# Kernel tuning notes

Measured on AMD Instinct MI355X. Metric: run time of the kernel, lower is better.

The kernel has to match this reference:

```python
import jax, jax.numpy as jnp
import numpy as np

B, N = 1, 768
C_A, C_S, C_Z = 768, 384, 128
H, C_HID, N_TRANS = 16, 48, 2
INF = 1e9
PNAMES = ['attn_s_ln_g', 'attn_ada_gate_w', 'attn_ada_gate_b', 'attn_ada_skip_w',
          'wq', 'bq', 'wk', 'wv', 'z_ln_g', 'z_ln_b', 'wb', 'wg', 'wo',
          'attn_out_gate_w', 'attn_out_gate_b',
          'tr_s_ln_g', 'tr_ada_gate_w', 'tr_ada_gate_b', 'tr_ada_skip_w',
          'tr_w1', 'tr_w2', 'tr_wo', 'tr_out_gate_w', 'tr_out_gate_b']


def _ln(x, eps=1e-5):
    mu = jnp.mean(x, axis=-1, keepdims=True)
    var = jnp.mean((x - mu) ** 2, axis=-1, keepdims=True)
    return (x - mu) * jax.lax.rsqrt(var + eps)


def _adaln(a, s, s_g, gate_w, gate_b, skip_w):
    # AF3 Algorithm 26 AdaLN: a <- LN(a, no affine); s <- LN(s, scale only)
    a_ln = _ln(a)
    s_ln = _ln(s) * s_g
    return jax.nn.sigmoid(s_ln @ gate_w + gate_b) * a_ln + s_ln @ skip_w


def setup_inputs() -> dict:
    key = jax.random.key(0)
    ks = iter(jax.random.split(key, 40))
    w = lambda *sh: jax.random.normal(next(ks), sh, jnp.float32) * 0.02
    return dict(
        a=jax.random.normal(next(ks), (B, N, C_A), jnp.float32),
        s=jax.random.normal(next(ks), (B, N, C_S), jnp.float32),
        z=jax.random.normal(next(ks), (B, N, N, C_Z), jnp.float32),
        mask=jnp.ones((B, N), jnp.int32),
        attn_s_ln_g=jnp.ones((C_S,), jnp.float32),
        attn_ada_gate_w=w(C_S, C_A),
        attn_ada_gate_b=jnp.zeros((C_A,), jnp.float32),
        attn_ada_skip_w=w(C_S, C_A),
        wq=w(C_A, H * C_HID), bq=jnp.zeros((H * C_HID,), jnp.float32),
        wk=w(C_A, H * C_HID), wv=w(C_A, H * C_HID),
        z_ln_g=jnp.ones((C_Z,), jnp.float32), z_ln_b=jnp.zeros((C_Z,), jnp.float32),
        wb=w(C_Z, H), wg=w(C_A, H * C_HID), wo=w(H * C_HID, C_A),
        attn_out_gate_w=w(C_S, C_A),
        attn_out_gate_b=jnp.full((C_A,), -2.0, jnp.float32),  # AdaLN-Zero bias init -2
        tr_s_ln_g=jnp.ones((C_S,), jnp.float32),
        tr_ada_gate_w=w(C_S, C_A),
        tr_ada_gate_b=jnp.zeros((C_A,), jnp.float32),
        tr_ada_skip_w=w(C_S, C_A),
        tr_w1=w(C_A, N_TRANS * C_A), tr_w2=w(C_A, N_TRANS * C_A),
        tr_wo=w(N_TRANS * C_A, C_A),
        tr_out_gate_w=w(C_S, C_A),
        tr_out_gate_b=jnp.full((C_A,), -2.0, jnp.float32),
    )


def _block(a, s, z, maskf, p):
    # --- AttentionPairBias (AF3 Alg 24), residual ---
    a_ln = _adaln(a, s, p['attn_s_ln_g'], p['attn_ada_gate_w'],
                  p['attn_ada_gate_b'], p['attn_ada_skip_w'])
    q = (a_ln @ p['wq'] + p['bq']).reshape(B, N, H, C_HID)
    k = (a_ln @ p['wk']).reshape(B, N, H, C_HID)
    v = (a_ln @ p['wv']).reshape(B, N, H, C_HID)
    pair_bias = (_ln(z) * p['z_ln_g'] + p['z_ln_b']) @ p['wb']  # [B,N,N,H]
    logits = jnp.einsum('bqhc,bkhc->bhqk', q, k) / np.float32(np.sqrt(C_HID))
    logits = logits + jnp.moveaxis(pair_bias, -1, 1)
    logits = logits + (maskf - 1.0)[:, None, None, :] * INF  # mask over keys
    attn = jax.nn.softmax(logits, axis=-1)
    o = jnp.einsum('bhqk,bkhc->bqhc', attn, v)
    g = jax.nn.sigmoid(a_ln @ p['wg']).reshape(B, N, H, C_HID)
    o = (o * g).reshape(B, N, H * C_HID) @ p['wo']
    o = jax.nn.sigmoid(s @ p['attn_out_gate_w'] + p['attn_out_gate_b']) * o
    a = a + o
    # --- ConditionedTransitionBlock (AF3 Alg 25, SwiGLU), residual ---
    t_ln = _adaln(a, s, p['tr_s_ln_g'], p['tr_ada_gate_w'],
                  p['tr_ada_gate_b'], p['tr_ada_skip_w'])
    hid = jax.nn.silu(t_ln @ p['tr_w1']) * (t_ln @ p['tr_w2'])
    t = jax.nn.sigmoid(s @ p['tr_out_gate_w'] + p['tr_out_gate_b']) * (hid @ p['tr_wo'])
    t = t * maskf[..., None]  # _mask_trans=True
    return a + t


def reference(a, s, z, mask, attn_s_ln_g, attn_ada_gate_w, attn_ada_gate_b,
              attn_ada_skip_w, wq, bq, wk, wv, z_ln_g, z_ln_b, wb, wg, wo,
              attn_out_gate_w, attn_out_gate_b, tr_s_ln_g, tr_ada_gate_w,
              tr_ada_gate_b, tr_ada_skip_w, tr_w1, tr_w2, tr_wo,
              tr_out_gate_w, tr_out_gate_b):
    p = dict(zip(PNAMES, (attn_s_ln_g, attn_ada_gate_w, attn_ada_gate_b,
                          attn_ada_skip_w, wq, bq, wk, wv, z_ln_g, z_ln_b, wb,
                          wg, wo, attn_out_gate_w, attn_out_gate_b, tr_s_ln_g,
                          tr_ada_gate_w, tr_ada_gate_b, tr_ada_skip_w, tr_w1,
                          tr_w2, tr_wo, tr_out_gate_w, tr_out_gate_b)))
    return _block(a, s, z, mask.astype(a.dtype), p)
```

## Files before the change

### kernel.cpp

```cpp
#include <hip/hip_runtime.h>
#include <hip/hip_bf16.h>
#include <stdint.h>


typedef __bf16 bf16x8 __attribute__((ext_vector_type(8)));
typedef float  f32x4  __attribute__((ext_vector_type(4)));

#define DEVI __device__ __forceinline__

DEVI uint16_t f2b(float f){ __hip_bfloat16 h = __float2bfloat16(f); return __builtin_bit_cast(uint16_t, h); }
DEVI float    b2f(uint16_t u){ return __bfloat162float(__builtin_bit_cast(__hip_bfloat16, u)); }
DEVI float    sigm(float x){ return 1.0f/(1.0f + __expf(-x)); }

DEVI f32x4 MFMA(uint4 a, uint4 b, f32x4 c){
  return __builtin_amdgcn_mfma_f32_16x16x32_bf16(
      __builtin_bit_cast(bf16x8, a), __builtin_bit_cast(bf16x8, b), c, 0, 0, 0);
}

DEVI void glds16(const void* g, void* l){
  __builtin_amdgcn_global_load_lds(
      (const __attribute__((address_space(1))) void*)g,
      (__attribute__((address_space(3))) void*)l, 16, 0, 0);
}

constexpr size_t SZ_BT_ADA   = (size_t)1536*384*2;
constexpr size_t OFF_BT_ADA_ATTN = 0;
constexpr size_t OFF_BT_ADA_TR   = OFF_BT_ADA_ATTN + SZ_BT_ADA;
constexpr size_t OFF_BT_OUTGATE  = OFF_BT_ADA_TR   + SZ_BT_ADA;
constexpr size_t OFF_BT_QKVG     = OFF_BT_OUTGATE  + SZ_BT_ADA;
constexpr size_t OFF_BT_WO       = OFF_BT_QKVG + (size_t)3072*768*2;
constexpr size_t OFF_BT_W12      = OFF_BT_WO   + (size_t)768*768*2;
constexpr size_t OFF_BT_TRWO     = OFF_BT_W12  + (size_t)3072*768*2;
constexpr size_t OFF_WBGT        = OFF_BT_TRWO + (size_t)768*1536*2;
constexpr size_t OFF_ZCOL        = OFF_WBGT + 4096;
constexpr size_t OFF_OGB         = OFF_ZCOL + 256;
constexpr size_t OFF_SBF         = OFF_OGB + 6144;
constexpr size_t OFF_SLNA        = OFF_SBF  + (size_t)768*384*2;
constexpr size_t OFF_SLNT        = OFF_SLNA + (size_t)768*384*2;
constexpr size_t OFF_GATEOUT     = OFF_SLNT + (size_t)768*384*2;
constexpr size_t OFF_LNA         = OFF_GATEOUT + (size_t)768*1536*4;
constexpr size_t OFF_GST         = OFF_LNA + (size_t)768*1536*4;
constexpr size_t OFF_ALNBF       = OFF_GST + (size_t)768*1536*4;
constexpr size_t OFF_QP          = OFF_ALNBF + (size_t)768*768*2;
constexpr size_t OFF_KP          = OFF_QP + (size_t)16*768*48*2;
constexpr size_t OFF_VT          = OFF_KP + (size_t)16*768*48*2;
constexpr size_t OFF_GB          = OFF_VT + (size_t)16*48*768*2;
constexpr size_t OFF_BIASB       = OFF_GB + (size_t)768*768*2;
constexpr size_t OFF_OBF         = OFF_BIASB + (size_t)16*768*768*2;
constexpr size_t OFF_AMID        = OFF_OBF + (size_t)768*768*2;
constexpr size_t OFF_HID         = OFF_BIASB;

extern "C" size_t kernel_workspace_size(void){ return (size_t)64 << 20; }

DEVI void cvt_body(const float* src, uint16_t* dst, int K, int N, int il, int local,
                   float (*lds)[33])
{
  int t = threadIdx.x;
  int tN = N >> 5;
  int n0 = (local % tN) << 5, k0 = (local / tN) << 5;
  int c = t & 31, r0 = t >> 5;
  #pragma unroll
  for (int i = 0; i < 4; i++){
    int kk = r0 + 8*i;
    lds[kk][c] = src[(size_t)(k0+kk)*N + n0 + c];
  }
  __syncthreads();
  int rbase = (il == 0) ? n0 : (((n0 >> 5) << 6) + ((il == 2) ? 32 : 0));
  #pragma unroll
  for (int i = 0; i < 4; i++){
    int nn = r0 + 8*i;
    dst[(size_t)(rbase+nn)*K + k0 + c] = f2b(lds[c][nn]);
  }
}

struct PreArgs {
  const float* src[6];
  uint16_t*    dst[6];
  int K[6], N[6], il[6];
  int prefix[7];
  int n_cvt;
  const float *s, *g_attn, *g_tr, *aogb, *togb, *zg, *zb, *wb, *ain;
  uint16_t *s_bf, *sln_a, *sln_t, *lna;
  float* ogb; uint16_t* wbgt; float* zcol;
};

__global__ __launch_bounds__(256) void k_pre(PreArgs a){
  __shared__ float lds[32][33];
  __shared__ float rs_[4], rq_[4];
  int bid = blockIdx.x, t = threadIdx.x;
  if (bid < a.n_cvt){
    int ti = 0;
    while (ti < 5 && bid >= a.prefix[ti+1]) ti++;
    cvt_body(a.src[ti], a.dst[ti], a.K[ti], a.N[ti], a.il[ti], bid - a.prefix[ti], lds);
    return;
  }
  int b = bid - a.n_cvt;
  if (b < 384){
    int row_id = b*2 + (t >> 7);
    int tt = t & 127;
    const float* row = a.s + (size_t)row_id*384;
    float x0 = row[tt], x1 = row[tt+128], x2 = row[tt+256];
    float sm = x0+x1+x2, sq = x0*x0+x1*x1+x2*x2;
    #pragma unroll
    for (int off = 32; off; off >>= 1){ sm += __shfl_xor(sm, off, 64); sq += __shfl_xor(sq, off, 64); }
    int w = t >> 6;
    if ((t & 63) == 0){ rs_[w] = sm; rq_[w] = sq; }
    __syncthreads();
    int base = (t >> 7)*2;
    float S = rs_[base]+rs_[base+1], Q = rq_[base]+rq_[base+1];
    float mu = S * (1.f/384.f);
    float var = Q * (1.f/384.f) - mu*mu;
    float rstd = rsqrtf(var + 1e-5f);
    float xs[3] = {x0, x1, x2};
    #pragma unroll
    for (int i = 0; i < 3; i++){
      int ci = tt + 128*i;
      float ln = (xs[i] - mu) * rstd;
      a.s_bf [(size_t)row_id*384 + ci] = f2b(xs[i]);
      a.sln_a[(size_t)row_id*384 + ci] = f2b(ln * a.g_attn[ci]);
      a.sln_t[(size_t)row_id*384 + ci] = f2b(ln * a.g_tr[ci]);
    }
  } else if (b == 384){
    for (int i = t; i < 1536; i += 256)
      a.ogb[i] = (i < 768) ? a.aogb[i] : a.togb[i-768];
  } else if (b == 385){
    for (int i = t; i < 2048; i += 256){
      int h = i >> 7, c = i & 127;
      a.wbgt[i] = f2b(a.zg[c] * a.wb[c*16 + h]);
    }
    if (t < 16){
      float cs = 0.f, cn = 0.f;
      for (int c = 0; c < 128; c++){ cs += a.zg[c]*a.wb[c*16+t]; cn += a.zb[c]*a.wb[c*16+t]; }
      a.zcol[t] = cs; a.zcol[16+t] = cn;
    }
  } else {
    int row = b - 386;
    const float* rp = a.ain + (size_t)row*768;
    float x0 = rp[t], x1 = rp[t+256], x2 = rp[t+512];
    float sm = x0+x1+x2, sq = x0*x0+x1*x1+x2*x2;
    #pragma unroll
    for (int off = 32; off; off >>= 1){ sm += __shfl_xor(sm, off, 64); sq += __shfl_xor(sq, off, 64); }
    int w = t >> 6;
    if ((t & 63) == 0){ rs_[w] = sm; rq_[w] = sq; }
    __syncthreads();
    float S = rs_[0]+rs_[1]+rs_[2]+rs_[3], Q = rq_[0]+rq_[1]+rq_[2]+rq_[3];
    float mu = S*(1.f/768.f), var = Q*(1.f/768.f) - mu*mu, rstd = rsqrtf(var + 1e-5f);
    float xs[3] = {x0, x1, x2};
    #pragma unroll
    for (int i = 0; i < 3; i++)
      a.lna[(size_t)row*768 + t + 256*i] = f2b((xs[i]-mu)*rstd);
  }
}

struct GemmP {
  const uint16_t *A, *BT;
  int N, K, gx, mode, gateLd, gateOff;
  float* outF; uint16_t* outB;
  const float *bias, *resid;
  const uint16_t *gate, *lna;
  const int* mask;
  uint16_t *qp, *kp, *vt, *gb;
  const float* bq;
};

DEVI void gemm_body(const GemmP& p, int bx, int by, uint16_t* As, uint16_t* Bs){
  int t = threadIdx.x;
  int n0 = bx*64, m0 = by*64;
  int w = t >> 6, lane = t & 63, mm = lane & 15, q = lane >> 4;
  const uint16_t* gA[4]; const uint16_t* gB[4];
  uint16_t* lA[4]; uint16_t* lB[4];
  #pragma unroll
  for (int i = 0; i < 4; i++){
    int fc = 256*w + 64*i + lane;
    int r = fc >> 4, cc = (fc & 15) ^ (r & 7);
    gA[i] = p.A  + (size_t)(m0 + r)*p.K + cc*8;
    gB[i] = p.BT + (size_t)(n0 + r)*p.K + cc*8;
    lA[i] = As + (256*w + 64*i)*8;
    lB[i] = Bs + (256*w + 64*i)*8;
  }
  f32x4 zz = {0.f,0.f,0.f,0.f};
  f32x4 acc[4] = {zz, zz, zz, zz};
  int sw = mm & 7;
  for (int k0 = 0; k0 < p.K; k0 += 128){
    __syncthreads();
    #pragma unroll
    for (int i = 0; i < 4; i++){
      glds16(gA[i] + k0, lA[i]);
      glds16(gB[i] + k0, lB[i]);
    }
    __syncthreads();
    #pragma unroll
    for (int kc = 0; kc < 4; kc++){
      uint4 av = *(const uint4*)&As[(16*w + mm)*128 + ((kc*4 + q) ^ sw)*8];
      #pragma unroll
      for (int j = 0; j < 4; j++){
        uint4 bv = *(const uint4*)&Bs[(16*j + mm)*128 + ((kc*4 + q) ^ sw)*8];
        acc[j] = MFMA(av, bv, acc[j]);
      }
    }
  }
  if (p.mode == 6){
    #pragma unroll
    for (int jj = 0; jj < 2; jj++){
      #pragma unroll
      for (int rr = 0; rr < 4; rr++){
        int row = m0 + 16*w + q*4 + rr;
        int col = (n0 >> 1) + 16*jj + mm;
        float x1 = acc[jj][rr], x2 = acc[jj+2][rr];
        p.outB[(size_t)row*(p.N >> 1) + col] = f2b(x1*sigm(x1)*x2);
      }
    }
    return;
  }
  if (p.mode == 8){
    #pragma unroll
    for (int jj = 0; jj < 2; jj++){
      #pragma unroll
      for (int rr = 0; rr < 4; rr++){
        int row = m0 + 16*w + q*4 + rr;
        int col = (n0 >> 1) + 16*jj + mm;
        float xg = acc[jj][rr], xs2 = acc[jj+2][rr];
        float ln = b2f(p.lna[(size_t)row*768 + col]);
        p.outB[(size_t)row*768 + col] = f2b(sigm(xg + p.bias[col])*ln + xs2);
      }
    }
    return;
  }
  if (p.mode == 7 && n0 >= 1536 && n0 < 2304){
    __syncthreads();
    #pragma unroll
    for (int j = 0; j < 4; j++)
      #pragma unroll
      for (int rr = 0; rr < 4; rr++)
        As[(16*j + mm)*72 + (16*w + q*4 + rr)] = f2b(acc[j][rr]);
    __syncthreads();
    int cl = t >> 2, ch = (t & 3)*16;
    int gc = n0 - 1536 + cl, h = gc/48, c = gc - 48*h;
    uint16_t* dst = p.vt + ((size_t)h*48 + c)*768 + m0 + ch;
    *(uint4*)dst       = *(const uint4*)&As[cl*72 + ch];
    *(uint4*)(dst + 8) = *(const uint4*)&As[cl*72 + ch + 8];
    return;
  }
  const float scale = 0.14433756729740643f;
  #pragma unroll
  for (int j = 0; j < 4; j++){
    #pragma unroll
    for (int rr = 0; rr < 4; rr++){
      int row = m0 + 16*w + q*4 + rr;
      int col = n0 + 16*j + mm;
      float v = acc[j][rr];
      size_t oi = (size_t)row*p.N + col;
      if (p.mode == 0)      p.outF[oi] = v;
      else if (p.mode == 1) p.outB[oi] = f2b(v);
      else if (p.mode == 3) p.outB[oi] = f2b(sigm(v + p.bias[col]));
      else if (p.mode == 5)
        p.outF[oi] = p.resid[oi] + b2f(p.gate[(size_t)row*p.gateLd + p.gateOff + col])*v;
      else if (p.mode == 4){
        float mf = (float)p.mask[row];
        p.outF[oi] = p.resid[oi] + mf * b2f(p.gate[(size_t)row*p.gateLd + p.gateOff + col]) * v;
      } else {
        if (col < 768){
          int h = col/48, c = col - h*48;
          p.qp[((size_t)h*768 + row)*48 + c] = f2b((v + p.bq[col])*scale);
        } else if (col < 1536){
          int cc = col - 768; int h = cc/48, c = cc - h*48;
          p.kp[((size_t)h*768 + row)*48 + c] = f2b(v);
        } else {
          p.gb[(size_t)row*768 + (col - 2304)] = f2b(v);
        }
      }
    }
  }
}

__global__ __launch_bounds__(256) void k_gemm(GemmP p){
  __shared__ __align__(16) uint16_t AsBs[2*64*128];
  gemm_body(p, blockIdx.x, blockIdx.y, AsBs, AsBs + 64*128);
}

DEVI void zbias_body(const float* __restrict__ z, const uint16_t* __restrict__ wbgt_g,
                     const float* __restrict__ zcol, uint16_t* __restrict__ bias_g,
                     int zbid, uint16_t* zb, uint16_t* wbt, float* mu_s, float* rs_s,
                     uint16_t* Sout)
{
  int t = threadIdx.x;
  int bx = zbid % 12, by = zbid / 12;
  size_t P0 = (size_t)by*768 + (size_t)bx*64;
  ((uint4*)wbt)[t] = ((const uint4*)wbgt_g)[t];
  int p = t >> 2, qq = t & 3;
  const float4* zp = (const float4*)(z + (P0 + p)*128) + qq*8;
  float s1 = 0.f, s2 = 0.f;
  uint32_t lb[16];
  #pragma unroll
  for (int it = 0; it < 8; it++){
    float4 v = zp[it];
    s1 += v.x + v.y + v.z + v.w;
    s2 += v.x*v.x + v.y*v.y + v.z*v.z + v.w*v.w;
    lb[2*it]   = (uint32_t)f2b(v.x) | ((uint32_t)f2b(v.y) << 16);
    lb[2*it+1] = (uint32_t)f2b(v.z) | ((uint32_t)f2b(v.w) << 16);
  }
  uint4* zb4 = (uint4*)zb;
  #pragma unroll
  for (int kk = 0; kk < 4; kk++)
    zb4[p*16 + qq*4 + kk] = ((uint4*)lb)[kk];
  s1 += __shfl_xor(s1, 1, 64); s1 += __shfl_xor(s1, 2, 64);
  s2 += __shfl_xor(s2, 1, 64); s2 += __shfl_xor(s2, 2, 64);
  if (qq == 0){
    float mu = s1 * (1.f/128.f);
    mu_s[p] = mu;
    rs_s[p] = rsqrtf(s2*(1.f/128.f) - mu*mu + 1e-5f);
  }
  __syncthreads();
  int w = t >> 6, lane = t & 63, hh = lane & 15, q = lane >> 4;
  float cs = zcol[hh], cn = zcol[16 + hh];
  f32x4 acc = {0.f, 0.f, 0.f, 0.f};
  const uint4* wbt4 = (const uint4*)wbt;
  #pragma unroll
  for (int kc = 0; kc < 4; kc++){
    uint4 av = zb4[(16*w + hh)*16 + kc*4 + q];
    uint4 bv = wbt4[hh*16 + kc*4 + q];
    acc = MFMA(av, bv, acc);
  }
  #pragma unroll
  for (int rr = 0; rr < 4; rr++){
    int pl = 16*w + q*4 + rr;
    float val = rs_s[pl]*(acc[rr] - mu_s[pl]*cs) + cn;
    Sout[hh*72 + pl] = f2b(val);
  }
  __syncthreads();
  int h2 = t >> 4, p2 = (t & 15)*4;
  uint2 v2 = *(uint2*)&Sout[h2*72 + p2];
  *(uint2*)(bias_g + (size_t)h2*589824 + P0 + p2) = v2;
}

struct ZbP { const float* z; const uint16_t* wbgt; const float* zcol; uint16_t* biasb; int off; };
struct CvtP {
  const float* src[8];
  uint16_t* dst[8];
  int K[8], N[8], il[8];
  int prefix[9];
  int n;
};
struct FatArgs {
  GemmP g[3];
  int gstart[4];
  int gn, gtotal, ztotal;
  ZbP zb;
  CvtP cv;
};

union __align__(16) MegaLds {
  struct { uint16_t As[64*128], Bs[64*128]; } g;
  struct { uint16_t zb[64*128]; uint16_t wbt[16*128]; float mu[64], rs[64]; uint16_t Sout[16*72]; } z;
  float cv[32][33];
};

__global__ __launch_bounds__(256) void k_mega(FatArgs fa){
  __shared__ MegaLds L;
  int bid = blockIdx.x;
  if (bid < fa.gtotal){
    int gi = 0;
    while (gi + 1 < fa.gn && bid >= fa.gstart[gi+1]) gi++;
    GemmP p = fa.g[gi];
    int local = bid - fa.gstart[gi];
    gemm_body(p, local % p.gx, local / p.gx, L.g.As, L.g.Bs);
    return;
  }
  if (bid < fa.gtotal + fa.ztotal){
    zbias_body(fa.zb.z, fa.zb.wbgt, fa.zb.zcol, fa.zb.biasb, fa.zb.off + (bid - fa.gtotal),
               L.z.zb, L.z.wbt, L.z.mu, L.z.rs, L.z.Sout);
    return;
  }
  int cid = bid - fa.gtotal - fa.ztotal;
  int ti = 0;
  while (ti + 1 < fa.cv.n && cid >= fa.cv.prefix[ti+1]) ti++;
  cvt_body(fa.cv.src[ti], fa.cv.dst[ti], fa.cv.K[ti], fa.cv.N[ti], fa.cv.il[ti],
           cid - fa.cv.prefix[ti], L.cv);
}

__global__ __launch_bounds__(256) void k_adaln2(
    const float* __restrict__ asrc, const uint16_t* __restrict__ gs,
    const float* __restrict__ gb, uint16_t* __restrict__ out)
{
  int b = blockIdx.x, t = threadIdx.x;
  const float* row = asrc + (size_t)b*768;
  float x0 = row[t], x1 = row[t+256], x2 = row[t+512];
  float sm = x0+x1+x2, sq = x0*x0+x1*x1+x2*x2;
  #pragma unroll
  for (int off = 32; off; off >>= 1){ sm += __shfl_xor(sm, off, 64); sq += __shfl_xor(sq, off, 64); }
  __shared__ float rs_[4], rq_[4];
  int w = t >> 6;
  if ((t & 63) == 0){ rs_[w] = sm; rq_[w] = sq; }
  __syncthreads();
  float S = rs_[0]+rs_[1]+rs_[2]+rs_[3], Q = rq_[0]+rq_[1]+rq_[2]+rq_[3];
  float mu = S*(1.f/768.f), var = Q*(1.f/768.f) - mu*mu, rstd = rsqrtf(var + 1e-5f);
  float xs[3] = {x0, x1, x2};
  #pragma unroll
  for (int i = 0; i < 3; i++){
    int c = t + 256*i;
    float g  = b2f(gs[(size_t)b*1536 + c]);
    float sk = b2f(gs[(size_t)b*1536 + 768 + c]);
    out[(size_t)b*768 + c] = f2b(sigm(g + gb[c]) * ((xs[i]-mu)*rstd) + sk);
  }
}

__global__ __launch_bounds__(256) void k_flash(
    const uint16_t* __restrict__ qp, const uint16_t* __restrict__ kp,
    const uint16_t* __restrict__ vt, const uint16_t* __restrict__ bias_g,
    const uint16_t* __restrict__ gb, const int* __restrict__ mask,
    uint16_t* __restrict__ obf)
{
  __shared__ __align__(16) uint16_t Qs[64*72], Ks[64*72], Vs[48*72], Ps[64*72], Bi[64*72];
  __shared__ float mk[768];
  int t = threadIdx.x;
  int q0 = blockIdx.x*64, h = blockIdx.y;
  int w = t >> 6, lane = t & 63, mm = lane & 15, q = lane >> 4;
  {
    const uint16_t* qbase = qp + ((size_t)h*768 + q0)*48;
    for (int i = t; i < 384; i += 256){
      int r = i/6, ch = i - r*6;
      *(uint4*)&Qs[r*72 + ch*8] = *(const uint4*)&qbase[r*48 + ch*8];
    }
    if (t < 128){
      uint4 z4; z4.x = z4.y = z4.z = z4.w = 0u;
      int r = t >> 1, off = 48 + (t & 1)*8;
      *(uint4*)&Qs[r*72 + off] = z4;
      *(uint4*)&Ks[r*72 + off] = z4;
    }
    mk[t] = (float)mask[t]; mk[t+256] = (float)mask[t+256]; mk[t+512] = (float)mask[t+512];
  }
  const uint16_t* sbase[5]; int sstep[5]; uint16_t* sdst[5];
  const uint16_t* bbase0 = bias_g + (size_t)h*589824 + (size_t)q0*768;
  #pragma unroll
  for (int i2 = 0; i2 < 5; i2++){
    int c = t + 256*i2;
    if (c < 384){
      int r = c/6, ch = c - 6*r;
      sbase[i2] = kp + ((size_t)h*768 + r)*48 + ch*8;
      sstep[i2] = 64*48;
      sdst[i2]  = &Ks[r*72 + ch*8];
    } else if (c < 768){
      int i3 = c - 384; int r = i3 >> 3, ch = i3 & 7;
      sbase[i2] = vt + ((size_t)h*48 + r)*768 + ch*8;
      sstep[i2] = 64;
      sdst[i2]  = &Vs[r*72 + ch*8];
    } else {
      int i3 = c - 768; int r = i3 >> 3, ch = i3 & 7;
      sbase[i2] = bbase0 + (size_t)r*768 + ch*8;
      sstep[i2] = 64;
      sdst[i2]  = &Bi[r*72 + ch*8];
    }
  }
  uint4 pre[5];
  #pragma unroll
  for (int i2 = 0; i2 < 5; i2++) pre[i2] = *(const uint4*)sbase[i2];

  f32x4 zz = {0.f,0.f,0.f,0.f};
  f32x4 o0 = zz, o1 = zz, o2 = zz;
  f32x4 m_i = {-1e30f,-1e30f,-1e30f,-1e30f};
  f32x4 l_i = zz;
  for (int kt = 0; kt < 12; kt++){
    __syncthreads();
    #pragma unroll
    for (int i2 = 0; i2 < 5; i2++) *(uint4*)sdst[i2] = pre[i2];
    __syncthreads();
    if (kt < 11){
      #pragma unroll
      for (int i2 = 0; i2 < 5; i2++)
        pre[i2] = *(const uint4*)(sbase[i2] + (size_t)(kt+1)*sstep[i2]);
    }
    f32x4 s[4] = {zz, zz, zz, zz};
    #pragma unroll
    for (int kc = 0; kc < 2; kc++){
      uint4 av = *(const uint4*)&Qs[(16*w + mm)*72 + kc*32 + q*8];
      #pragma unroll
      for (int j = 0; j < 4; j++){
        uint4 bv = *(const uint4*)&Ks[(16*j + mm)*72 + kc*32 + q*8];
        s[j] = MFMA(av, bv, s[j]);
      }
    }
    int rbase = 16*w + q*4;
    #pragma unroll
    for (int j = 0; j < 4; j++){
      int scol = kt*64 + 16*j + mm;
      float mt = (mk[scol] - 1.f)*1e9f;
      #pragma unroll
      for (int rr = 0; rr < 4; rr++)
        s[j][rr] += b2f(Bi[(rbase+rr)*72 + 16*j + mm]) + mt;
    }
    f32x4 tm = s[0];
    #pragma unroll
    for (int j = 1; j < 4; j++)
      #pragma unroll
      for (int rr = 0; rr < 4; rr++) tm[rr] = fmaxf(tm[rr], s[j][rr]);
    #pragma unroll
    for (int off = 1; off < 16; off <<= 1)
      #pragma unroll
      for (int rr = 0; rr < 4; rr++) tm[rr] = fmaxf(tm[rr], __shfl_xor(tm[rr], off, 64));
    f32x4 mnew, alpha, rsum = zz;
    #pragma unroll
    for (int rr = 0; rr < 4; rr++){
      mnew[rr] = fmaxf(m_i[rr], tm[rr]);
      alpha[rr] = __expf(m_i[rr] - mnew[rr]);
    }
    #pragma unroll
    for (int j = 0; j < 4; j++)
      #pragma unroll
      for (int rr = 0; rr < 4; rr++){
        s[j][rr] = __expf(s[j][rr] - mnew[rr]);
        rsum[rr] += s[j][rr];
      }
    #pragma unroll
    for (int off = 1; off < 16; off <<= 1)
      #pragma unroll
      for (int rr = 0; rr < 4; rr++) rsum[rr] += __shfl_xor(rsum[rr], off, 64);
    #pragma unroll
    for (int rr = 0; rr < 4; rr++){
      l_i[rr] = l_i[rr]*alpha[rr] + rsum[rr];
      o0[rr] *= alpha[rr]; o1[rr] *= alpha[rr]; o2[rr] *= alpha[rr];
      m_i[rr] = mnew[rr];
    }
    #pragma unroll
    for (int j = 0; j < 4; j++)
      #pragma unroll
      for (int rr = 0; rr < 4; rr++)
        Ps[(16*w + q*4 + rr)*72 + 16*j + mm] = f2b(s[j][rr]);
    __syncthreads();
    #pragma unroll
    for (int kc = 0; kc < 2; kc++){
      uint4 av = *(const uint4*)&Ps[(16*w + mm)*72 + kc*32 + q*8];
      uint4 bv0 = *(const uint4*)&Vs[(mm)*72      + kc*32 + q*8];
      uint4 bv1 = *(const uint4*)&Vs[(16+mm)*72   + kc*32 + q*8];
      uint4 bv2 = *(const uint4*)&Vs[(32+mm)*72   + kc*32 + q*8];
      o0 = MFMA(av, bv0, o0);
      o1 = MFMA(av, bv1, o1);
      o2 = MFMA(av, bv2, o2);
    }
  }
  f32x4 inv;
  #pragma unroll
  for (int rr = 0; rr < 4; rr++) inv[rr] = 1.f / l_i[rr];
  #pragma unroll
  for (int j = 0; j < 3; j++){
    f32x4 ov = (j == 0) ? o0 : (j == 1) ? o1 : o2;
    int col = 16*j + mm;
    #pragma unroll
    for (int rr = 0; rr < 4; rr++){
      int row = q0 + 16*w + q*4 + rr;
      float g = b2f(gb[(size_t)row*768 + h*48 + col]);
      obf[(size_t)row*768 + h*48 + col] = f2b(ov[rr]*inv[rr]*sigm(g));
    }
  }
}

extern "C" void kernel_launch(void* const* d_in, const int* in_sizes, int n_in,
                              void* d_out, int out_size, void* d_ws, size_t ws_size,
                              hipStream_t stream)
{
  const float* a            = (const float*)d_in[0];
  const float* s            = (const float*)d_in[1];
  const float* z            = (const float*)d_in[2];
  const int*   mask         = (const int*)  d_in[3];
  const float* attn_s_ln_g  = (const float*)d_in[4];
  const float* attn_gate_w  = (const float*)d_in[5];
  const float* attn_gate_b  = (const float*)d_in[6];
  const float* attn_skip_w  = (const float*)d_in[7];
  const float* wq           = (const float*)d_in[8];
  const float* bq           = (const float*)d_in[9];
  const float* wk           = (const float*)d_in[10];
  const float* wv           = (const float*)d_in[11];
  const float* z_ln_g       = (const float*)d_in[12];
  const float* z_ln_b       = (const float*)d_in[13];
  const float* wb           = (const float*)d_in[14];
  const float* wg           = (const float*)d_in[15];
  const float* wo           = (const float*)d_in[16];
  const float* attn_og_w    = (const float*)d_in[17];
  const float* attn_og_b    = (const float*)d_in[18];
  const float* tr_s_ln_g    = (const float*)d_in[19];
  const float* tr_gate_w    = (const float*)d_in[20];
  const float* tr_gate_b    = (const float*)d_in[21];
  const float* tr_skip_w    = (const float*)d_in[22];
  const float* tr_w1        = (const float*)d_in[23];
  const float* tr_w2        = (const float*)d_in[24];
  const float* tr_wo        = (const float*)d_in[25];
  const float* tr_og_w      = (const float*)d_in[26];
  const float* tr_og_b      = (const float*)d_in[27];

  char* wsb = (char*)d_ws;
  uint16_t* BTa   = (uint16_t*)(wsb + OFF_BT_ADA_ATTN);
  uint16_t* BTt   = (uint16_t*)(wsb + OFF_BT_ADA_TR);
  uint16_t* BTo   = (uint16_t*)(wsb + OFF_BT_OUTGATE);
  uint16_t* BTq   = (uint16_t*)(wsb + OFF_BT_QKVG);
  uint16_t* BTwo  = (uint16_t*)(wsb + OFF_BT_WO);
  uint16_t* BTw12 = (uint16_t*)(wsb + OFF_BT_W12);
  uint16_t* BTtw  = (uint16_t*)(wsb + OFF_BT_TRWO);
  uint16_t* WBGT  = (uint16_t*)(wsb + OFF_WBGT);
  float*    ZCOL  = (float*)   (wsb + OFF_ZCOL);
  float*    OGB   = (float*)   (wsb + OFF_OGB);
  uint16_t* SBF   = (uint16_t*)(wsb + OFF_SBF);
  uint16_t* SLNA  = (uint16_t*)(wsb + OFF_SLNA);
  uint16_t* SLNT  = (uint16_t*)(wsb + OFF_SLNT);
  uint16_t* GATEOUTB = (uint16_t*)(wsb + OFF_GATEOUT);
  uint16_t* LNABF = (uint16_t*)(wsb + OFF_LNA);
  uint16_t* GSTB  = (uint16_t*)(wsb + OFF_GST);
  uint16_t* ALNBF = (uint16_t*)(wsb + OFF_ALNBF);
  uint16_t* QP    = (uint16_t*)(wsb + OFF_QP);
  uint16_t* KP    = (uint16_t*)(wsb + OFF_KP);
  uint16_t* VT    = (uint16_t*)(wsb + OFF_VT);
  uint16_t* GB    = (uint16_t*)(wsb + OFF_GB);
  uint16_t* BIASB = (uint16_t*)(wsb + OFF_BIASB);
  uint16_t* OBF   = (uint16_t*)(wsb + OFF_OBF);
  float*    AMID  = (float*)   (wsb + OFF_AMID);
  uint16_t* HIDBF = (uint16_t*)(wsb + OFF_HID);
  float*    OUTF  = (float*)d_out;

  PreArgs pa;
  {
    const float* srcs[6] = {attn_gate_w, attn_skip_w, tr_gate_w, tr_skip_w, attn_og_w, tr_og_w};
    uint16_t* dsts[6] = {BTa, BTa, BTt, BTt + (size_t)768*384,
                         BTo, BTo + (size_t)768*384};
    int ils[6] = {1, 2, 0, 0, 0, 0};
    int pre = 0;
    for (int i = 0; i < 6; i++){
      pa.src[i] = srcs[i]; pa.dst[i] = dsts[i]; pa.K[i] = 384; pa.N[i] = 768; pa.il[i] = ils[i];
      pa.prefix[i] = pre; pre += 288;
    }
    pa.prefix[6] = pre;
    pa.n_cvt = pre;
  }
  pa.s = s; pa.g_attn = attn_s_ln_g; pa.g_tr = tr_s_ln_g;
  pa.aogb = attn_og_b; pa.togb = tr_og_b;
  pa.zg = z_ln_g; pa.zb = z_ln_b; pa.wb = wb; pa.ain = a;
  pa.s_bf = SBF; pa.sln_a = SLNA; pa.sln_t = SLNT; pa.lna = LNABF;
  pa.ogb = OGB; pa.wbgt = WBGT; pa.zcol = ZCOL;
  k_pre<<<pa.n_cvt + 386 + 768, 256, 0, stream>>>(pa);

  FatArgs f2{};
  {
    GemmP p{};
    p.A = SBF; p.BT = BTo; p.N = 1536; p.K = 384; p.gx = 24; p.mode = 3;
    p.outB = GATEOUTB; p.bias = OGB;
    f2.g[0] = p;
    p = GemmP{};
    p.A = SLNA; p.BT = BTa; p.N = 1536; p.K = 384; p.gx = 24; p.mode = 8;
    p.outB = ALNBF; p.bias = attn_gate_b; p.lna = LNABF;
    f2.g[1] = p;
    p = GemmP{};
    p.A = SLNT; p.BT = BTt; p.N = 1536; p.K = 384; p.gx = 24; p.mode = 1; p.outB = GSTB;
    f2.g[2] = p;
    f2.gstart[0] = 0; f2.gstart[1] = 288; f2.gstart[2] = 576; f2.gstart[3] = 864;
    f2.gn = 3; f2.gtotal = 864;
    f2.ztotal = 4608;
    f2.zb = ZbP{z, WBGT, ZCOL, BIASB, 0};
    const float* csrc[8] = {wq, wk, wv, wg, wo, tr_w1, tr_w2, tr_wo};
    uint16_t* cdst[8] = {BTq, BTq + (size_t)768*768, BTq + (size_t)2*768*768, BTq + (size_t)3*768*768,
                         BTwo, BTw12, BTw12, BTtw};
    int cK[8] = {768,768,768,768,768, 768,768, 1536};
    int cN[8] = {768,768,768,768,768, 1536,1536, 768};
    int cil[8] = {0,0,0,0,0, 1,2, 0};
    int ct[8]  = {576,576,576,576,576, 1152,1152, 1152};
    int cpre = 0;
    for (int i = 0; i < 8; i++){
      f2.cv.src[i] = csrc[i]; f2.cv.dst[i] = cdst[i];
      f2.cv.K[i] = cK[i]; f2.cv.N[i] = cN[i]; f2.cv.il[i] = cil[i];
      f2.cv.prefix[i] = cpre; cpre += ct[i];
    }
    f2.cv.prefix[8] = cpre;
    f2.cv.n = 8;
    k_mega<<<864 + 4608 + cpre, 256, 0, stream>>>(f2);
  }

  FatArgs f4{};
  {
    GemmP p{};
    p.A = ALNBF; p.BT = BTq; p.N = 3072; p.K = 768; p.gx = 48; p.mode = 7;
    p.qp = QP; p.kp = KP; p.vt = VT; p.gb = GB; p.bq = bq;
    f4.g[0] = p;
    f4.gstart[0] = 0; f4.gstart[1] = 576; f4.gn = 1; f4.gtotal = 576;
    f4.ztotal = 4608;
    f4.zb = ZbP{z, WBGT, ZCOL, BIASB, 4608};
    f4.cv.n = 0;
    k_mega<<<576 + 4608, 256, 0, stream>>>(f4);
  }

  k_flash<<<dim3(12,16), 256, 0, stream>>>(QP, KP, VT, BIASB, GB, mask, OBF);

  {
    GemmP p{};
    p.A = OBF; p.BT = BTwo; p.N = 768; p.K = 768; p.gx = 12; p.mode = 5;
    p.outF = AMID; p.gate = GATEOUTB; p.gateLd = 1536; p.gateOff = 0; p.resid = a;
    k_gemm<<<dim3(12,12), 256, 0, stream>>>(p);
  }

  k_adaln2<<<768, 256, 0, stream>>>(AMID, GSTB, tr_gate_b, ALNBF);

  {
    GemmP p{};
    p.A = ALNBF; p.BT = BTw12; p.N = 3072; p.K = 768; p.gx = 48; p.mode = 6;
    p.outB = HIDBF;
    k_gemm<<<dim3(48,12), 256, 0, stream>>>(p);
  }

  {
    GemmP p{};
    p.A = HIDBF; p.BT = BTtw; p.N = 768; p.K = 1536; p.gx = 12; p.mode = 4;
    p.outF = OUTF; p.gate = GATEOUTB; p.gateLd = 1536; p.gateOff = 768;
    p.resid = AMID; p.mask = mask;
    k_gemm<<<dim3(12,12), 256, 0, stream>>>(p);
  }
}
```

Measured before the change: 578.7 us.

## Merge flash, gemms and adaLN tail into one cooperative persistent kernel

Replaces the five tail launches (flash attention, output-projection gemm, adaLN, SwiGLU gemm, transition output gemm) with a single cooperative kernel that separates the stages with grid-wide syncs, keeping the old launches as a fallback. The aim is to remove per-launch overhead and inter-kernel gaps. In exchange, grid.sync has its own cost, the grid size is capped by occupancy, and the LDS union sized for the largest stage may lower occupancy for the small adaLN stage.

```diff
diff --git a/kernel.cpp b/kernel.cpp
--- a/kernel.cpp
+++ b/kernel.cpp
@@ -1,6 +1,9 @@
 #include <hip/hip_runtime.h>
 #include <hip/hip_bf16.h>
+#include <hip/hip_cooperative_groups.h>
 #include <stdint.h>
+
+namespace cg = cooperative_groups;
 
 
 typedef __bf16 bf16x8 __attribute__((ext_vector_type(8)));
@@ -378,17 +381,15 @@
            cid - fa.cv.prefix[ti], L.cv);
 }
 
-__global__ __launch_bounds__(256) void k_adaln2(
-    const float* __restrict__ asrc, const uint16_t* __restrict__ gs,
-    const float* __restrict__ gb, uint16_t* __restrict__ out)
+DEVI void adaln_body(const float* asrc, const uint16_t* gs, const float* gb,
+                     uint16_t* out, int b, float* rs_, float* rq_)
 {
-  int b = blockIdx.x, t = threadIdx.x;
+  int t = threadIdx.x;
   const float* row = asrc + (size_t)b*768;
   float x0 = row[t], x1 = row[t+256], x2 = row[t+512];
   float sm = x0+x1+x2, sq = x0*x0+x1*x1+x2*x2;
   #pragma unroll
   for (int off = 32; off; off >>= 1){ sm += __shfl_xor(sm, off, 64); sq += __shfl_xor(sq, off, 64); }
-  __shared__ float rs_[4], rq_[4];
   int w = t >> 6;
   if ((t & 63) == 0){ rs_[w] = sm; rq_[w] = sq; }
   __syncthreads();
@@ -404,19 +405,29 @@
   }
 }
 
-__global__ __launch_bounds__(256) void k_flash(
-    const uint16_t* __restrict__ qp, const uint16_t* __restrict__ kp,
-    const uint16_t* __restrict__ vt, const uint16_t* __restrict__ bias_g,
-    const uint16_t* __restrict__ gb, const int* __restrict__ mask,
-    uint16_t* __restrict__ obf)
+__global__ __launch_bounds__(256) void k_adaln2(
+    const float* __restrict__ asrc, const uint16_t* __restrict__ gs,
+    const float* __restrict__ gb, uint16_t* __restrict__ out)
 {
-  __shared__ __align__(16) uint16_t Qs[64*72], Ks[64*72], Vs[48*72], Ps[64*72], Bi[64*72];
-  __shared__ float mk[768];
+  __shared__ float rs_[4], rq_[4];
+  adaln_body(asrc, gs, gb, out, blockIdx.x, rs_, rq_);
+}
+
+struct FlashP {
+  const uint16_t *qp, *kp, *vt, *biasb, *gb;
+  const int* mask;
+  uint16_t* obf;
+};
+
+DEVI void flash_body(const FlashP& fp, int bx, int h,
+                     uint16_t* Qs, uint16_t* Ks, uint16_t* Vs, uint16_t* Ps,
+                     uint16_t* Bi, float* mk)
+{
   int t = threadIdx.x;
-  int q0 = blockIdx.x*64, h = blockIdx.y;
+  int q0 = bx*64;
   int w = t >> 6, lane = t & 63, mm = lane & 15, q = lane >> 4;
   {
-    const uint16_t* qbase = qp + ((size_t)h*768 + q0)*48;
+    const uint16_t* qbase = fp.qp + ((size_t)h*768 + q0)*48;
     for (int i = t; i < 384; i += 256){
       int r = i/6, ch = i - r*6;
       *(uint4*)&Qs[r*72 + ch*8] = *(const uint4*)&qbase[r*48 + ch*8];
@@ -427,21 +438,21 @@
       *(uint4*)&Qs[r*72 + off] = z4;
       *(uint4*)&Ks[r*72 + off] = z4;
     }
-    mk[t] = (float)mask[t]; mk[t+256] = (float)mask[t+256]; mk[t+512] = (float)mask[t+512];
+    mk[t] = (float)fp.mask[t]; mk[t+256] = (float)fp.mask[t+256]; mk[t+512] = (float)fp.mask[t+512];
   }
   const uint16_t* sbase[5]; int sstep[5]; uint16_t* sdst[5];
-  const uint16_t* bbase0 = bias_g + (size_t)h*589824 + (size_t)q0*768;
+  const uint16_t* bbase0 = fp.biasb + (size_t)h*589824 + (size_t)q0*768;
   #pragma unroll
   for (int i2 = 0; i2 < 5; i2++){
     int c = t + 256*i2;
     if (c < 384){
       int r = c/6, ch = c - 6*r;
-      sbase[i2] = kp + ((size_t)h*768 + r)*48 + ch*8;
+      sbase[i2] = fp.kp + ((size_t)h*768 + r)*48 + ch*8;
       sstep[i2] = 64*48;
       sdst[i2]  = &Ks[r*72 + ch*8];
     } else if (c < 768){
       int i3 = c - 384; int r = i3 >> 3, ch = i3 & 7;
-      sbase[i2] = vt + ((size_t)h*48 + r)*768 + ch*8;
+      sbase[i2] = fp.vt + ((size_t)h*48 + r)*768 + ch*8;
       sstep[i2] = 64;
       sdst[i2]  = &Vs[r*72 + ch*8];
     } else {
@@ -547,10 +558,50 @@
     #pragma unroll
     for (int rr = 0; rr < 4; rr++){
       int row = q0 + 16*w + q*4 + rr;
-      float g = b2f(gb[(size_t)row*768 + h*48 + col]);
-      obf[(size_t)row*768 + h*48 + col] = f2b(ov[rr]*inv[rr]*sigm(g));
-    }
-  }
+      float g = b2f(fp.gb[(size_t)row*768 + h*48 + col]);
+      fp.obf[(size_t)row*768 + h*48 + col] = f2b(ov[rr]*inv[rr]*sigm(g));
+    }
+  }
+}
+
+__global__ __launch_bounds__(256) void k_flash(FlashP fp){
+  __shared__ __align__(16) uint16_t Qs[64*72], Ks[64*72], Vs[48*72], Ps[64*72], Bi[64*72];
+  __shared__ float mk[768];
+  flash_body(fp, blockIdx.x, blockIdx.y, Qs, Ks, Vs, Ps, Bi, mk);
+}
+
+struct TailArgs {
+  FlashP fl;
+  GemmP g5, g7, g8;
+  const float* amid; const uint16_t* gst; const float* trgb; uint16_t* alnbf;
+};
+
+union __align__(16) TailLds {
+  struct { uint16_t Qs[64*72], Ks[64*72], Vs[48*72], Ps[64*72], Bi[64*72]; float mk[768]; } f;
+  struct { uint16_t As[64*128], Bs[64*128]; } g;
+  struct { float rs_[4], rq_[4]; } a;
+};
+
+__global__ __launch_bounds__(256) void k_tail(TailArgs ta){
+  __shared__ TailLds L;
+  cg::grid_group grid = cg::this_grid();
+  int bid = blockIdx.x, nb = gridDim.x;
+  for (int v = bid; v < 192; v += nb)
+    flash_body(ta.fl, v % 12, v / 12, L.f.Qs, L.f.Ks, L.f.Vs, L.f.Ps, L.f.Bi, L.f.mk);
+  grid.sync();
+  for (int v = bid; v < 144; v += nb)
+    gemm_body(ta.g5, v % 12, v / 12, L.g.As, L.g.Bs);
+  grid.sync();
+  for (int v = bid; v < 768; v += nb){
+    adaln_body(ta.amid, ta.gst, ta.trgb, ta.alnbf, v, L.a.rs_, L.a.rq_);
+    __syncthreads();
+  }
+  grid.sync();
+  for (int v = bid; v < 576; v += nb)
+    gemm_body(ta.g7, v % 48, v / 48, L.g.As, L.g.Bs);
+  grid.sync();
+  for (int v = bid; v < 144; v += nb)
+    gemm_body(ta.g8, v % 12, v / 12, L.g.As, L.g.Bs);
 }
 
 extern "C" void kernel_launch(void* const* d_in, const int* in_sizes, int n_in,
@@ -683,29 +734,38 @@
     k_mega<<<576 + 4608, 256, 0, stream>>>(f4);
   }
 
-  k_flash<<<dim3(12,16), 256, 0, stream>>>(QP, KP, VT, BIASB, GB, mask, OBF);
-
+  TailArgs ta{};
+  ta.fl = FlashP{QP, KP, VT, BIASB, GB, mask, OBF};
   {
     GemmP p{};
     p.A = OBF; p.BT = BTwo; p.N = 768; p.K = 768; p.gx = 12; p.mode = 5;
     p.outF = AMID; p.gate = GATEOUTB; p.gateLd = 1536; p.gateOff = 0; p.resid = a;
-    k_gemm<<<dim3(12,12), 256, 0, stream>>>(p);
-  }
-
-  k_adaln2<<<768, 256, 0, stream>>>(AMID, GSTB, tr_gate_b, ALNBF);
-
-  {
-    GemmP p{};
+    ta.g5 = p;
+    p = GemmP{};
     p.A = ALNBF; p.BT = BTw12; p.N = 3072; p.K = 768; p.gx = 48; p.mode = 6;
     p.outB = HIDBF;
-    k_gemm<<<dim3(48,12), 256, 0, stream>>>(p);
-  }
-
-  {
-    GemmP p{};
+    ta.g7 = p;
+    p = GemmP{};
     p.A = HIDBF; p.BT = BTtw; p.N = 768; p.K = 1536; p.gx = 12; p.mode = 4;
     p.outF = OUTF; p.gate = GATEOUTB; p.gateLd = 1536; p.gateOff = 768;
     p.resid = AMID; p.mask = mask;
-    k_gemm<<<dim3(12,12), 256, 0, stream>>>(p);
-  }
-}
+    ta.g8 = p;
+  }
+  ta.amid = AMID; ta.gst = GSTB; ta.trgb = tr_gate_b; ta.alnbf = ALNBF;
+
+  int maxb = 0;
+  hipError_t qe = hipOccupancyMaxActiveBlocksPerMultiprocessor(&maxb, k_tail, 256, 0);
+  int tgrid = (qe == hipSuccess && maxb > 0) ? maxb * 256 : 512;
+  if (tgrid > 768) tgrid = 768;
+  if (tgrid < 192) tgrid = 192;
+  void* targs[] = { &ta };
+  hipError_t le = hipLaunchCooperativeKernel(reinterpret_cast<void*>(k_tail),
+                                             dim3(tgrid), dim3(256), targs, 0, stream);
+  if (le != hipSuccess){
+    k_flash<<<dim3(12,16), 256, 0, stream>>>(ta.fl);
+    k_gemm<<<dim3(12,12), 256, 0, stream>>>(ta.g5);
+    k_adaln2<<<768, 256, 0, stream>>>(AMID, GSTB, tr_gate_b, ALNBF);
+    k_gemm<<<dim3(48,12), 256, 0, stream>>>(ta.g7);
+    k_gemm<<<dim3(12,12), 256, 0, stream>>>(ta.g8);
+  }
+}
```

After: 751.3 us. +29.8%, slower.
